# Kernel tuning notes

Hardware: AMD Instinct MI355X
Metric: run time of the kernel (lower is better)

## Reference

```python
import jax, jax.numpy as jnp
import numpy as np

# ---- config (from DAREConfig init_kwargs) ----
TAU = 0.1
RHO_VIS = 0.5          # is_visual=True -> rho_target = rho_vis_target
PREFIX_KAPPA = 64
LAMBDA_RATIO = 1.0
LAMBDA_SOFT = 0.1
LAMBDA_HARD = 1.0

B, S = 256, 32768


def setup_inputs() -> dict:
    key = jax.random.key(0)
    k1, k2 = jax.random.split(key)
    importance = jax.random.normal(k1, (B, S), dtype=jnp.float32)
    modality_mask = jax.random.randint(k2, (B, S), 0, 2) > 0  # bool [B,S]
    return {"importance": importance, "modality_mask": modality_mask}


def reference(importance, modality_mask):
    """Vectorized DAREController.route(is_visual=True, training=True).

    The torch loop over batch with data-dependent k is replaced by a
    per-row k-th-largest threshold: for each row, k_b = min(int(rho*|mm_b|),
    |valid_b|); tokens with score >= k_b-th largest valid score are kept
    (this matches DifferentiableTopK's hard mask soft>0.5, i.e. exactly the
    top-k scores, assuming no ties).
    """
    mm = modality_mask.astype(bool)          # [B,S]
    b, s = importance.shape

    target = jnp.clip(mm.sum(axis=1).astype(jnp.float32) * RHO_VIS, 1.0)  # [B]
    prefix = jnp.arange(s) < min(PREFIX_KAPPA, s)                          # [S]
    eff = mm & ~prefix[None, :]                                            # [B,S] routable tokens
    n_valid = eff.sum(axis=1)                                              # [B]
    k = jnp.minimum(target.astype(jnp.int32), n_valid)                     # [B] per-row top-k size

    neg_inf = jnp.float32(-jnp.inf)
    masked = jnp.where(eff, importance, neg_inf)                           # [B,S]
    sorted_desc = -jnp.sort(-masked, axis=1)                               # [B,S]
    idx = jnp.clip(k - 1, 0, s - 1)                                        # [B]
    thresh = jnp.take_along_axis(sorted_desc, idx[:, None], axis=1)        # [B,1]
    hard = masked >= thresh                                                # top-k of valid tokens

    keep_mask = prefix[None, :] | (hard & (k > 0)[:, None])                # [B,S]

    # ---- training / is_visual losses ----
    kept = (keep_mask & mm).sum(axis=1).astype(jnp.float32)
    denom = mm.sum(axis=1).astype(jnp.float32) + 1e-6
    actual_ratio = kept / denom
    loss_ratio = jnp.mean(jnp.abs(actual_ratio - RHO_VIS))                 # F.l1_loss

    dropped = mm & ~keep_mask
    n_drop = dropped.sum()
    drop_mean = jnp.sum(jnp.where(dropped, importance, 0.0)) / jnp.maximum(n_drop, 1).astype(jnp.float32)
    loss_soft = jnp.where(n_drop > 0, drop_mean, 0.0)

    loss_hard = jnp.mean(jnp.clip(RHO_VIS - actual_ratio, 0.0))

    return (keep_mask,
            LAMBDA_RATIO * loss_ratio,
            LAMBDA_SOFT * loss_soft,
            LAMBDA_HARD * loss_hard)
```

## Files before the change

### kernel.cpp

```cpp
#include <hip/hip_runtime.h>


#define NB 256
#define NS 32768
#define KAPPA 64
#define NT 1024
#define NW (NT / 64)
#define V4 (NS / NT / 4)

typedef float f32x4 __attribute__((ext_vector_type(4)));
typedef int   i32x4 __attribute__((ext_vector_type(4)));
typedef unsigned int u32;

__device__ __forceinline__ u32 fkey(float f) {
    u32 u = __float_as_uint(f);
    return (u & 0x80000000u) ? ~u : (u | 0x80000000u);
}

__global__ __launch_bounds__(NT) void dare_rows(const float* __restrict__ imp,
                                                const int* __restrict__ mask,
                                                float* __restrict__ keep,
                                                float* __restrict__ stats) {
    __shared__ float simp[NS];
    __shared__ u32 hist[256];
    __shared__ u32 wtot[4];
    __shared__ u32 wred_mm[NW], wred_eff[NW];
    __shared__ u32 sh_mm, sh_eff, sh_pref, sh_rem;
    __shared__ u32 sh_kept, sh_ndrop;
    __shared__ float sh_dsum;

    const int row = blockIdx.x;
    const int tid = threadIdx.x;
    const int lane = tid & 63;
    const int wid = tid >> 6;
    const f32x4* rimp4  = (const f32x4*)(imp  + (size_t)row * NS);
    const i32x4* rmask4 = (const i32x4*)(mask + (size_t)row * NS);
    f32x4*       rkeep4 = (f32x4*)      (keep + (size_t)row * NS);

    if (tid < 256) hist[tid] = 0;
    if (tid == 0) { sh_pref = 0; sh_rem = 1; sh_kept = 0; sh_ndrop = 0; sh_dsum = 0.0f; }

    #pragma unroll
    for (int i = 0; i < V4; i++) {
        const int idx4 = tid + i * NT;
        __builtin_amdgcn_global_load_lds(
            (const __attribute__((address_space(1))) u32*)(&rimp4[idx4]),
            (__attribute__((address_space(3))) u32*)(&simp[idx4 * 4]),
            16, 0, 0);
    }

    i32x4 mv[V4];
    #pragma unroll
    for (int i = 0; i < V4; i++) mv[i] = rmask4[tid + i * NT];

    u32 mmbits = 0, effbits = 0;
    #pragma unroll
    for (int i = 0; i < V4; i++) {
        const int idx4 = tid + i * NT;
        #pragma unroll
        for (int j = 0; j < 4; j++) {
            const int e = i * 4 + j;
            const int col = idx4 * 4 + j;
            const bool mm  = (mv[i][j] != 0);
            const bool eff = mm && (col >= KAPPA);
            mmbits  |= (mm  ? 1u : 0u) << e;
            effbits |= (eff ? 1u : 0u) << e;
        }
    }
    int mm_local  = __popc(mmbits);
    int eff_local = __popc(effbits);
    #pragma unroll
    for (int off = 32; off; off >>= 1) {
        mm_local  += __shfl_down(mm_local, off);
        eff_local += __shfl_down(eff_local, off);
    }
    if (lane == 0) { wred_mm[wid] = (u32)mm_local; wred_eff[wid] = (u32)eff_local; }

    __syncthreads();

    #pragma unroll
    for (int i = 0; i < V4; i++) {
        const int idx4 = tid + i * NT;
        const f32x4 v = *(const f32x4*)&simp[idx4 * 4];
        #pragma unroll
        for (int j = 0; j < 4; j++) {
            if ((effbits >> (i * 4 + j)) & 1u) atomicAdd(&hist[fkey(v[j]) >> 24], 1u);
        }
    }
    if (tid == 0) {
        u32 sm = 0, se = 0;
        #pragma unroll
        for (int w = 0; w < NW; w++) { sm += wred_mm[w]; se += wred_eff[w]; }
        sh_mm = sm; sh_eff = se;
    }
    __syncthreads();

    #pragma unroll
    for (int pass = 0; pass < 4; pass++) {
        const int shift = 24 - 8 * pass;

        if (pass > 0) {
            if (tid < 256) hist[tid] = 0;
            __syncthreads();
            const u32 pmask = 0xFFFFFFFFu << (shift + 8);
            const u32 pref = sh_pref;
            #pragma unroll
            for (int i = 0; i < V4; i++) {
                const int idx4 = tid + i * NT;
                const f32x4 v = *(const f32x4*)&simp[idx4 * 4];
                #pragma unroll
                for (int j = 0; j < 4; j++) {
                    const u32 key = fkey(v[j]);
                    const bool match = ((effbits >> (i * 4 + j)) & 1u) && ((key & pmask) == pref);
                    if (match) atomicAdd(&hist[(key >> shift) & 0xFFu], 1u);
                }
            }
            __syncthreads();
        }

        u32 h = 0, s = 0;
        if (tid < 256) {
            h = hist[tid];
            s = h;
            #pragma unroll
            for (int off = 1; off < 64; off <<= 1) {
                const u32 t = __shfl_down(s, off);
                if (lane + off < 64) s += t;
            }
            if (lane == 0) wtot[tid >> 6] = s;
        }
        __syncthreads();
        if (tid < 256) {
            u32 sfull = s;
            for (int w = (tid >> 6) + 1; w < 4; w++) sfull += wtot[w];
            u32 rem;
            if (pass == 0) {
                const float target = fmaxf((float)sh_mm * 0.5f, 1.0f);
                const int k = min((int)target, (int)sh_eff);
                rem = (u32)max(k, 1);
            } else {
                rem = sh_rem;
            }
            if (sfull >= rem && (sfull - h) < rem) {
                sh_pref = (pass == 0) ? ((u32)tid << 24) : (sh_pref | ((u32)tid << shift));
                sh_rem = rem - (sfull - h);
            }
        }
        __syncthreads();
    }

    const u32 thresh = sh_pref;
    const bool kpos = (sh_eff > 0);

    int kept_l = 0, ndrop_l = 0;
    float dsum_l = 0.0f;
    #pragma unroll
    for (int i = 0; i < V4; i++) {
        const int idx4 = tid + i * NT;
        const f32x4 v = *(const f32x4*)&simp[idx4 * 4];
        f32x4 o;
        #pragma unroll
        for (int j = 0; j < 4; j++) {
            const int e = i * 4 + j;
            const int col = idx4 * 4 + j;
            const bool mm  = (mmbits >> e) & 1u;
            const bool eff = (effbits >> e) & 1u;
            const bool hard = kpos && eff && (fkey(v[j]) >= thresh);
            const bool kp = (col < KAPPA) || hard;
            o[j] = kp ? 1.0f : 0.0f;
            kept_l += (kp && mm) ? 1 : 0;
            const bool drop = mm && !kp;
            ndrop_l += drop ? 1 : 0;
            dsum_l += drop ? v[j] : 0.0f;
        }
        rkeep4[idx4] = o;
    }
    #pragma unroll
    for (int off = 32; off; off >>= 1) {
        kept_l  += __shfl_down(kept_l, off);
        ndrop_l += __shfl_down(ndrop_l, off);
        dsum_l  += __shfl_down(dsum_l, off);
    }
    if (lane == 0) {
        atomicAdd(&sh_kept,  (u32)kept_l);
        atomicAdd(&sh_ndrop, (u32)ndrop_l);
        atomicAdd(&sh_dsum,  dsum_l);
    }
    __syncthreads();
    if (tid == 0) {
        stats[row * 4 + 0] = (float)sh_kept;
        stats[row * 4 + 1] = (float)sh_mm;
        stats[row * 4 + 2] = (float)sh_ndrop;
        stats[row * 4 + 3] = sh_dsum;
    }
}

__global__ __launch_bounds__(256) void dare_losses(const float* __restrict__ stats,
                                                   float* __restrict__ out) {
    __shared__ float w_a[4], w_h[4], w_n[4], w_d[4];
    const int tid = threadIdx.x;
    const float kept = stats[tid * 4 + 0];
    const float mmc  = stats[tid * 4 + 1];
    const float nd   = stats[tid * 4 + 2];
    const float ds   = stats[tid * 4 + 3];
    const float ratio = kept / (mmc + 1e-6f);
    float a = fabsf(ratio - 0.5f);
    float h = fmaxf(0.5f - ratio, 0.0f);
    float n = nd, d = ds;
    #pragma unroll
    for (int off = 32; off; off >>= 1) {
        a += __shfl_down(a, off);
        h += __shfl_down(h, off);
        n += __shfl_down(n, off);
        d += __shfl_down(d, off);
    }
    const int wid = tid >> 6, lane = tid & 63;
    if (lane == 0) { w_a[wid] = a; w_h[wid] = h; w_n[wid] = n; w_d[wid] = d; }
    __syncthreads();
    if (tid == 0) {
        float sa = 0.f, shh = 0.f, sn = 0.f, sd = 0.f;
        for (int w = 0; w < 4; w++) { sa += w_a[w]; shh += w_h[w]; sn += w_n[w]; sd += w_d[w]; }
        out[0] = sa / (float)NB;
        out[1] = (sn > 0.0f) ? 0.1f * (sd / fmaxf(sn, 1.0f)) : 0.0f;
        out[2] = shh / (float)NB;
    }
}

extern "C" void kernel_launch(void* const* d_in, const int* in_sizes, int n_in,
                              void* d_out, int out_size, void* d_ws, size_t ws_size,
                              hipStream_t stream) {
    const float* imp  = (const float*)d_in[0];
    const int*   mask = (const int*)d_in[1];
    float* out   = (float*)d_out;
    float* stats = (float*)d_ws;

    dare_rows<<<NB, NT, 0, stream>>>(imp, mask, out, stats);
    dare_losses<<<1, 256, 0, stream>>>(stats, out + (size_t)NB * NS);
}
```

Before: 118.8 us.

## Replace four-pass radix select with 11-bit histogram plus candidate bit-select

The 4-pass 8-bit radix select over the whole row becomes one 2048-bin histogram pass. It is followed by compacting the candidates in the chosen bin into shared memory and resolving the remaining 21 bits with a single wave using ballot/popcount. The mask is also staged through LDS via global_load_lds instead of register loads, and shared memory is reused for the importance values. This cuts three full-row LDS scans and atomics passes. In exchange it adds more serialized single-wave work and a slow fallback when the bin overflows the candidate buffer.

```diff
diff --git a/kernel.cpp b/kernel.cpp
--- a/kernel.cpp
+++ b/kernel.cpp
@@ -5,8 +5,11 @@
 #define NS 32768
 #define KAPPA 64
 #define NT 1024
-#define NW (NT / 64)
 #define V4 (NS / NT / 4)
+#define NBIN 2048
+#define NSEG 256
+#define SEGW (NBIN / NSEG)
+#define CAND_CAP 4096
 
 typedef float f32x4 __attribute__((ext_vector_type(4)));
 typedef int   i32x4 __attribute__((ext_vector_type(4)));
@@ -21,52 +24,57 @@
                                                 const int* __restrict__ mask,
                                                 float* __restrict__ keep,
                                                 float* __restrict__ stats) {
-    __shared__ float simp[NS];
-    __shared__ u32 hist[256];
+    __shared__ float K[NS];
+    __shared__ u32 hist[NBIN];
+    __shared__ u32 cand[CAND_CAP];
+    __shared__ u32 bm_eff[NT];
     __shared__ u32 wtot[4];
-    __shared__ u32 wred_mm[NW], wred_eff[NW];
-    __shared__ u32 sh_mm, sh_eff, sh_pref, sh_rem;
+    __shared__ u32 sh_mm, sh_eff, sh_cand;
+    __shared__ u32 sh_b0, sh_rem, sh_thresh;
     __shared__ u32 sh_kept, sh_ndrop;
     __shared__ float sh_dsum;
 
     const int row = blockIdx.x;
     const int tid = threadIdx.x;
     const int lane = tid & 63;
-    const int wid = tid >> 6;
     const f32x4* rimp4  = (const f32x4*)(imp  + (size_t)row * NS);
     const i32x4* rmask4 = (const i32x4*)(mask + (size_t)row * NS);
     f32x4*       rkeep4 = (f32x4*)      (keep + (size_t)row * NS);
 
-    if (tid < 256) hist[tid] = 0;
-    if (tid == 0) { sh_pref = 0; sh_rem = 1; sh_kept = 0; sh_ndrop = 0; sh_dsum = 0.0f; }
-
     #pragma unroll
     for (int i = 0; i < V4; i++) {
         const int idx4 = tid + i * NT;
         __builtin_amdgcn_global_load_lds(
-            (const __attribute__((address_space(1))) u32*)(&rimp4[idx4]),
-            (__attribute__((address_space(3))) u32*)(&simp[idx4 * 4]),
+            (const __attribute__((address_space(1))) u32*)(&rmask4[idx4]),
+            (__attribute__((address_space(3))) u32*)(&K[idx4 * 4]),
             16, 0, 0);
     }
-
-    i32x4 mv[V4];
-    #pragma unroll
-    for (int i = 0; i < V4; i++) mv[i] = rmask4[tid + i * NT];
-
+    hist[tid] = 0;
+    hist[tid + NT] = 0;
+    if (tid == 0) {
+        sh_mm = 0; sh_eff = 0; sh_cand = 0;
+        sh_b0 = 0; sh_rem = 1; sh_thresh = 0;
+        sh_kept = 0; sh_ndrop = 0; sh_dsum = 0.0f;
+    }
+    __syncthreads();
+
+    const i32x4* Km = (const i32x4*)K;
     u32 mmbits = 0, effbits = 0;
     #pragma unroll
     for (int i = 0; i < V4; i++) {
         const int idx4 = tid + i * NT;
+        const i32x4 m = Km[idx4];
         #pragma unroll
         for (int j = 0; j < 4; j++) {
             const int e = i * 4 + j;
             const int col = idx4 * 4 + j;
-            const bool mm  = (mv[i][j] != 0);
+            const bool mm  = (m[j] != 0);
             const bool eff = mm && (col >= KAPPA);
             mmbits  |= (mm  ? 1u : 0u) << e;
             effbits |= (eff ? 1u : 0u) << e;
         }
     }
+    bm_eff[tid] = effbits;
     int mm_local  = __popc(mmbits);
     int eff_local = __popc(effbits);
     #pragma unroll
@@ -74,90 +82,132 @@
         mm_local  += __shfl_down(mm_local, off);
         eff_local += __shfl_down(eff_local, off);
     }
-    if (lane == 0) { wred_mm[wid] = (u32)mm_local; wred_eff[wid] = (u32)eff_local; }
-
-    __syncthreads();
-
-    #pragma unroll
-    for (int i = 0; i < V4; i++) {
-        const int idx4 = tid + i * NT;
-        const f32x4 v = *(const f32x4*)&simp[idx4 * 4];
+    if (lane == 0) {
+        atomicAdd(&sh_mm,  (u32)mm_local);
+        atomicAdd(&sh_eff, (u32)eff_local);
+    }
+    __syncthreads();
+
+    #pragma unroll
+    for (int i = 0; i < V4; i++) {
+        const int idx4 = tid + i * NT;
+        __builtin_amdgcn_global_load_lds(
+            (const __attribute__((address_space(1))) u32*)(&rimp4[idx4]),
+            (__attribute__((address_space(3))) u32*)(&K[idx4 * 4]),
+            16, 0, 0);
+    }
+    __syncthreads();
+
+    const f32x4* Kf = (const f32x4*)K;
+    #pragma unroll
+    for (int i = 0; i < V4; i++) {
+        const int idx4 = tid + i * NT;
+        const f32x4 v = Kf[idx4];
         #pragma unroll
         for (int j = 0; j < 4; j++) {
-            if ((effbits >> (i * 4 + j)) & 1u) atomicAdd(&hist[fkey(v[j]) >> 24], 1u);
-        }
-    }
-    if (tid == 0) {
-        u32 sm = 0, se = 0;
-        #pragma unroll
-        for (int w = 0; w < NW; w++) { sm += wred_mm[w]; se += wred_eff[w]; }
-        sh_mm = sm; sh_eff = se;
-    }
-    __syncthreads();
-
-    #pragma unroll
-    for (int pass = 0; pass < 4; pass++) {
-        const int shift = 24 - 8 * pass;
-
-        if (pass > 0) {
-            if (tid < 256) hist[tid] = 0;
-            __syncthreads();
-            const u32 pmask = 0xFFFFFFFFu << (shift + 8);
-            const u32 pref = sh_pref;
+            if ((effbits >> (i * 4 + j)) & 1u) atomicAdd(&hist[fkey(v[j]) >> 21], 1u);
+        }
+    }
+    __syncthreads();
+
+    u32 r[SEGW];
+    u32 hsum = 0, s = 0;
+    if (tid < NSEG) {
+        #pragma unroll
+        for (int b = 0; b < SEGW; b++) { r[b] = hist[tid * SEGW + b]; hsum += r[b]; }
+        s = hsum;
+        #pragma unroll
+        for (int off = 1; off < 64; off <<= 1) {
+            const u32 t = __shfl_down(s, off);
+            if (lane + off < 64) s += t;
+        }
+        if (lane == 0) wtot[tid >> 6] = s;
+    }
+    __syncthreads();
+    if (tid < NSEG) {
+        u32 sfull = s;
+        for (int w = (tid >> 6) + 1; w < 4; w++) sfull += wtot[w];
+        const float target = fmaxf((float)sh_mm * 0.5f, 1.0f);
+        const int k = min((int)target, (int)sh_eff);
+        const u32 rem = (u32)max(k, 1);
+        const u32 above = sfull - hsum;
+        if (sfull >= rem && above < rem) {
+            u32 cum = above;
             #pragma unroll
-            for (int i = 0; i < V4; i++) {
-                const int idx4 = tid + i * NT;
-                const f32x4 v = *(const f32x4*)&simp[idx4 * 4];
-                #pragma unroll
-                for (int j = 0; j < 4; j++) {
+            for (int b = SEGW - 1; b >= 0; b--) {
+                if (cum + r[b] >= rem) { sh_b0 = tid * SEGW + b; sh_rem = rem - cum; break; }
+                cum += r[b];
+            }
+        }
+    }
+    __syncthreads();
+
+    const u32 b0 = sh_b0;
+    const bool kpos = (sh_eff > 0);
+    if (kpos) {
+        #pragma unroll
+        for (int i = 0; i < V4; i++) {
+            const int idx4 = tid + i * NT;
+            const f32x4 v = Kf[idx4];
+            #pragma unroll
+            for (int j = 0; j < 4; j++) {
+                if ((effbits >> (i * 4 + j)) & 1u) {
                     const u32 key = fkey(v[j]);
-                    const bool match = ((effbits >> (i * 4 + j)) & 1u) && ((key & pmask) == pref);
-                    if (match) atomicAdd(&hist[(key >> shift) & 0xFFu], 1u);
+                    if ((key >> 21) == b0) {
+                        const u32 pos = atomicAdd(&sh_cand, 1u);
+                        if (pos < CAND_CAP) cand[pos] = key;
+                    }
                 }
             }
-            __syncthreads();
-        }
-
-        u32 h = 0, s = 0;
-        if (tid < 256) {
-            h = hist[tid];
-            s = h;
-            #pragma unroll
-            for (int off = 1; off < 64; off <<= 1) {
-                const u32 t = __shfl_down(s, off);
-                if (lane + off < 64) s += t;
-            }
-            if (lane == 0) wtot[tid >> 6] = s;
-        }
-        __syncthreads();
-        if (tid < 256) {
-            u32 sfull = s;
-            for (int w = (tid >> 6) + 1; w < 4; w++) sfull += wtot[w];
-            u32 rem;
-            if (pass == 0) {
-                const float target = fmaxf((float)sh_mm * 0.5f, 1.0f);
-                const int k = min((int)target, (int)sh_eff);
-                rem = (u32)max(k, 1);
-            } else {
-                rem = sh_rem;
-            }
-            if (sfull >= rem && (sfull - h) < rem) {
-                sh_pref = (pass == 0) ? ((u32)tid << 24) : (sh_pref | ((u32)tid << shift));
-                sh_rem = rem - (sfull - h);
-            }
-        }
-        __syncthreads();
-    }
-
-    const u32 thresh = sh_pref;
-    const bool kpos = (sh_eff > 0);
-
+        }
+    }
+    __syncthreads();
+
+    if (tid < 64 && kpos) {
+        const u32 total = sh_cand;
+        if (total > 0 && total <= CAND_CAP) {
+            u32 rem = sh_rem, pref = 0;
+            const int slots = (int)((total + 63u) >> 6);
+            for (int bit = 20; bit >= 0; bit--) {
+                u32 c1 = 0;
+                for (int sl = 0; sl < slots; sl++) {
+                    const u32 idx = (u32)lane + ((u32)sl << 6);
+                    const u32 lw = (idx < total) ? (cand[idx] & 0x1FFFFFu) : 0xFFFFFFFFu;
+                    const bool m = (lw >> (bit + 1)) == (pref >> (bit + 1)) && ((lw >> bit) & 1u);
+                    c1 += (u32)__popcll(__ballot(m));
+                }
+                if (c1 >= rem) pref |= 1u << bit; else rem -= c1;
+            }
+            if (lane == 0) sh_thresh = (b0 << 21) | pref;
+        } else if (total > CAND_CAP) {
+            u32 rem = sh_rem, pref = 0;
+            for (int bit = 20; bit >= 0; bit--) {
+                u32 c1 = 0;
+                for (int p = lane; p < NS; p += 64) {
+                    const int idx4 = p >> 2;
+                    const u32 eb = bm_eff[idx4 & (NT - 1)];
+                    const int e = ((idx4 >> 10) << 2) | (p & 3);
+                    const u32 key = fkey(K[p]);
+                    const bool effb = (eb >> e) & 1u;
+                    const bool m = effb && ((key >> 21) == b0) &&
+                                   ((key & 0x1FFFFFu) >> (bit + 1)) == (pref >> (bit + 1)) &&
+                                   ((key >> bit) & 1u);
+                    c1 += (u32)__popcll(__ballot(m));
+                }
+                if (c1 >= rem) pref |= 1u << bit; else rem -= c1;
+            }
+            if (lane == 0) sh_thresh = (b0 << 21) | pref;
+        }
+    }
+    __syncthreads();
+
+    const u32 thresh = sh_thresh;
     int kept_l = 0, ndrop_l = 0;
     float dsum_l = 0.0f;
     #pragma unroll
     for (int i = 0; i < V4; i++) {
         const int idx4 = tid + i * NT;
-        const f32x4 v = *(const f32x4*)&simp[idx4 * 4];
+        const f32x4 v = Kf[idx4];
         f32x4 o;
         #pragma unroll
         for (int j = 0; j < 4; j++) {
```

New measurement: 113.6 us. -4.4%, faster.
